# Kernel tuning notes

Hardware: AMD Instinct MI355X
Metric: run time of the kernel (lower is better)

The kernel has to match this reference:

```python
import jax, jax.numpy as jnp
import numpy as np

S, E, H, D, F = 2048, 1280, 16, 80, 5120
EPS = 1e-6


def _ln(x, g, b):
    m = x.mean(-1, keepdims=True)
    v = x.var(-1, keepdims=True)
    return (x - m) * jax.lax.rsqrt(v + EPS) * g + b


def _rotate_half(x):
    x1, x2 = jnp.split(x, 2, axis=-1)
    return jnp.concatenate([-x2, x1], axis=-1)


def _quick_gelu(x):
    return x * jax.nn.sigmoid(1.702 * x)


def setup_inputs() -> dict:
    key = jax.random.key(0)
    ks = jax.random.split(key, 12)
    inp = {
        "hidden_states": jax.random.normal(ks[0], (S, E), jnp.float32),
        "attention_mask": jnp.ones((1, 1, S, S), jnp.bool_),
        "cos": jax.random.uniform(ks[1], (S, D), jnp.float32),
        "sin": jax.random.uniform(ks[2], (S, D), jnp.float32),
        "ln1_g": jnp.ones((E,), jnp.float32),
        "ln1_b": jnp.zeros((E,), jnp.float32),
        "ln2_g": jnp.ones((E,), jnp.float32),
        "ln2_b": jnp.zeros((E,), jnp.float32),
        "w_qkv": jax.random.normal(ks[3], (E, 3 * E), jnp.float32) * (E ** -0.5),
        "b_qkv": jax.random.normal(ks[4], (3 * E,), jnp.float32) * 0.02,
        "w_o": jax.random.normal(ks[5], (E, E), jnp.float32) * (E ** -0.5),
        "b_o": jax.random.normal(ks[6], (E,), jnp.float32) * 0.02,
        "w_fc1": jax.random.normal(ks[7], (E, F), jnp.float32) * (E ** -0.5),
        "b_fc1": jax.random.normal(ks[8], (F,), jnp.float32) * 0.02,
        "w_fc2": jax.random.normal(ks[9], (F, E), jnp.float32) * (F ** -0.5),
        "b_fc2": jax.random.normal(ks[10], (E,), jnp.float32) * 0.02,
    }
    return inp


def reference(hidden_states, attention_mask, cos, sin, ln1_g, ln1_b, ln2_g, ln2_b,
              w_qkv, b_qkv, w_o, b_o, w_fc1, b_fc1, w_fc2, b_fc2):
    x = hidden_states  # [S, E]
    h = _ln(x, ln1_g, ln1_b)
    qkv = h @ w_qkv + b_qkv  # [S, 3E]
    q, k, v = jnp.split(qkv, 3, axis=-1)
    q = q.reshape(S, H, D)
    k = k.reshape(S, H, D)
    v = v.reshape(S, H, D)
    # rotary in fp32, cos/sin broadcast over head axis: [S, 1, D]
    c = cos[:, None, :].astype(jnp.float32)
    s = sin[:, None, :].astype(jnp.float32)
    qf, kf = q.astype(jnp.float32), k.astype(jnp.float32)
    q = (qf * c + _rotate_half(qf) * s).astype(q.dtype)
    k = (kf * c + _rotate_half(kf) * s).astype(k.dtype)
    # attention scores [H, S, S]
    scores = jnp.einsum('shd,thd->hst', q, k) / np.float32(np.sqrt(D))
    scores = jnp.where(attention_mask[0], scores, jnp.finfo(scores.dtype).min)
    probs = jax.nn.softmax(scores.astype(jnp.float32), axis=-1).astype(q.dtype)
    attn = jnp.einsum('hst,thd->shd', probs, v).reshape(S, E)
    attn = attn @ w_o + b_o
    x = x + attn
    h2 = _ln(x, ln2_g, ln2_b)
    mlp = _quick_gelu(h2 @ w_fc1 + b_fc1) @ w_fc2 + b_fc2
    return x + mlp
```

## Files before the change

kernel.cpp:

```cpp
#include <hip/hip_runtime.h>
#include <stdint.h>
#include <math.h>

#define S_LEN 2048
#define EMB   1280
#define NHEAD 16
#define HDIM  80
#define FDIM  5120

typedef __bf16 bf16x8 __attribute__((ext_vector_type(8)));
typedef float  f32x4  __attribute__((ext_vector_type(4)));
typedef int    i32x4  __attribute__((ext_vector_type(4)));
typedef unsigned short u16x8 __attribute__((ext_vector_type(8)));
typedef unsigned short u16x4 __attribute__((ext_vector_type(4)));

__device__ __forceinline__ float b2f(unsigned short u) {
    union { float f; unsigned int i; } x; x.i = ((unsigned int)u) << 16; return x.f;
}
__device__ __forceinline__ unsigned short f2b(float f) {
    union { float f; unsigned int i; } x; x.f = f;
    unsigned int r = x.i + 0x7FFFu + ((x.i >> 16) & 1u);
    return (unsigned short)(r >> 16);
}

__device__ __forceinline__ float wave_rsum(float v) {
    #pragma unroll
    for (int o = 32; o; o >>= 1) v += __shfl_down(v, o);
    return v;
}

__device__ __forceinline__ void trans64(
    const float* __restrict__ in, unsigned short* __restrict__ out,
    int R, int C, int bx, int by, int tid)
{
    __shared__ unsigned short tile[64][65];
    int c0 = bx * 64, r0 = by * 64;
    int tx = tid & 63, ty = tid >> 6;
    #pragma unroll
    for (int j = 0; j < 16; ++j) {
        int row = ty + j * 4;
        tile[row][tx] = f2b(in[(size_t)(r0 + row) * C + c0 + tx]);
    }
    __syncthreads();
    #pragma unroll
    for (int j = 0; j < 16; ++j) {
        int row = ty + j * 4;
        out[(size_t)(c0 + row) * R + r0 + tx] = tile[tx][row];
    }
}

__global__ __launch_bounds__(256) void transpose4_kernel(
    const float* __restrict__ w_qkv, unsigned short* __restrict__ wT_qkv,
    const float* __restrict__ w_o,   unsigned short* __restrict__ wT_o,
    const float* __restrict__ w_fc1, unsigned short* __restrict__ wT_fc1,
    const float* __restrict__ w_fc2, unsigned short* __restrict__ wT_fc2)
{
    int id = blockIdx.x, tid = threadIdx.x;
    if (id < 1200) {
        trans64(w_qkv, wT_qkv, 1280, 3840, id % 60, id / 60, tid);
    } else if (id < 1600) {
        int t = id - 1200;
        trans64(w_o, wT_o, 1280, 1280, t % 20, t / 20, tid);
    } else if (id < 3200) {
        int t = id - 1600;
        trans64(w_fc1, wT_fc1, 1280, 5120, t % 80, t / 80, tid);
    } else {
        int t = id - 3200;
        trans64(w_fc2, wT_fc2, 5120, 1280, t % 20, t / 20, tid);
    }
}

__global__ __launch_bounds__(256) void ln_kernel(
    const float* __restrict__ x,
    const float* __restrict__ g,
    const float* __restrict__ b,
    unsigned short* __restrict__ out)
{
    int row = blockIdx.x, tid = threadIdx.x;
    int lane = tid & 63, wave = tid >> 6;
    const float* xr = x + (size_t)row * EMB;
    float v[5], s = 0.f, ss = 0.f;
    #pragma unroll
    for (int i = 0; i < 5; ++i) {
        float f = xr[tid + i * 256];
        v[i] = f; s += f; ss += f * f;
    }
    s = wave_rsum(s); ss = wave_rsum(ss);
    __shared__ float rs[4], rss[4];
    if (lane == 0) { rs[wave] = s; rss[wave] = ss; }
    __syncthreads();
    float st  = rs[0] + rs[1] + rs[2] + rs[3];
    float sst = rss[0] + rss[1] + rss[2] + rss[3];
    float mean = st * (1.0f / EMB);
    float var  = sst * (1.0f / EMB) - mean * mean;
    float inv  = rsqrtf(var + 1e-6f);
    unsigned short* orow = out + (size_t)row * EMB;
    #pragma unroll
    for (int i = 0; i < 5; ++i) {
        int c = tid + i * 256;
        orow[c] = f2b((v[i] - mean) * inv * g[c] + b[c]);
    }
}

__global__ __launch_bounds__(256) void addbias_kernel(
    const float* __restrict__ res,
    const float* __restrict__ bias,
    float* __restrict__ out)
{
    size_t i4 = ((size_t)blockIdx.x * 256 + threadIdx.x) * 4;
    f32x4 a = *(const f32x4*)&res[i4];
    f32x4 bv = *(const f32x4*)&bias[(int)(i4 % EMB)];
    *(f32x4*)&out[i4] = a + bv;
}

template<int EPI, int OM, int SPLIT>
__global__ __launch_bounds__(256) void gemm_kernel(
    const unsigned short* __restrict__ A,
    const unsigned short* __restrict__ Bt,
    const float* __restrict__ bias,
    void* __restrict__ Cv,
    int M, int N, int K)
{
    __shared__ __align__(16) unsigned short As[2][128 * 32];
    __shared__ __align__(16) unsigned short Bs[2][128 * 32];

    int tid = threadIdx.x;
    int lane = tid & 63, wave = tid >> 6;

    int gx = gridDim.x, gy = gridDim.y;
    int nwg = gx * gy * gridDim.z;
    int flat = blockIdx.x + gx * (blockIdx.y + gy * blockIdx.z);
    int cpx = nwg >> 3;
    int logical = (flat & 7) * cpx + (flat >> 3);
    int bx = logical % gx;
    int rem = logical / gx;
    int by = rem % gy;
    int bz = rem / gy;

    int m0 = bx * 128, n0 = by * 128;
    int wm = (wave >> 1) * 64, wn = (wave & 1) * 64;
    int kc = K / SPLIT;
    int kbeg = bz * kc;
    const int NITER = kc / 32;

    f32x4 acc[4][4];
    #pragma unroll
    for (int i = 0; i < 4; ++i)
        #pragma unroll
        for (int j = 0; j < 4; ++j)
            acc[i][j] = (f32x4){0.f, 0.f, 0.f, 0.f};

    int u = tid ^ ((tid >> 3) & 7);
    const unsigned short* Ap0 = A  + (size_t)(m0 + (u >> 2)) * K + (u & 3) * 8 + kbeg;
    const unsigned short* Ap1 = Ap0 + (size_t)64 * K;
    const unsigned short* Bp0 = Bt + (size_t)(n0 + (u >> 2)) * K + (u & 3) * 8 + kbeg;
    const unsigned short* Bp1 = Bp0 + (size_t)64 * K;

    int arow = lane & 15, aq = (lane >> 4) * 8;
    int aswz = ((arow >> 1) & 7) << 3;
    int aoff[4], boff[4];
    #pragma unroll
    for (int i = 0; i < 4; ++i) {
        aoff[i] = ((wm + i * 16 + arow) * 32 + aq) ^ aswz;
        boff[i] = ((wn + i * 16 + arow) * 32 + aq) ^ aswz;
    }

    i32x4 rA0a, rA1a, rB0a, rB1a, rA0b, rA1b, rB0b, rB1b;

    rA0b = *(const i32x4*)(Ap0);
    rA1b = *(const i32x4*)(Ap1);
    rB0b = *(const i32x4*)(Bp0);
    rB1b = *(const i32x4*)(Bp1);
    *(i32x4*)&As[0][tid * 8]        = rA0b;
    *(i32x4*)&As[0][2048 + tid * 8] = rA1b;
    *(i32x4*)&Bs[0][tid * 8]        = rB0b;
    *(i32x4*)&Bs[0][2048 + tid * 8] = rB1b;
    if (NITER > 1) {
        rA0a = *(const i32x4*)(Ap0 + 32);
        rA1a = *(const i32x4*)(Ap1 + 32);
        rB0a = *(const i32x4*)(Bp0 + 32);
        rB1a = *(const i32x4*)(Bp1 + 32);
    }
    __syncthreads();

#define GSTEP(IT, AW0, AW1, BW0, BW1, AL0, AL1, BL0, BL1)                    \
    {                                                                         \
        const int cur = (IT) & 1, nb = cur ^ 1;                               \
        if ((IT) + 1 < NITER) {                                               \
            *(i32x4*)&As[nb][tid * 8]        = AW0;                           \
            *(i32x4*)&As[nb][2048 + tid * 8] = AW1;                           \
            *(i32x4*)&Bs[nb][tid * 8]        = BW0;                           \
            *(i32x4*)&Bs[nb][2048 + tid * 8] = BW1;                           \
        }                                                                     \
        if ((IT) + 2 < NITER) {                                               \
            int ko = ((IT) + 2) * 32;                                         \
            AL0 = *(const i32x4*)(Ap0 + ko);                                  \
            AL1 = *(const i32x4*)(Ap1 + ko);                                  \
            BL0 = *(const i32x4*)(Bp0 + ko);                                  \
            BL1 = *(const i32x4*)(Bp1 + ko);                                  \
        }                                                                     \
        bf16x8 af[4], bfm[4];                                                 \
        _Pragma("unroll") for (int i = 0; i < 4; ++i) {                       \
            af[i]  = *(const bf16x8*)&As[cur][aoff[i]];                       \
            bfm[i] = *(const bf16x8*)&Bs[cur][boff[i]];                       \
        }                                                                     \
        _Pragma("unroll") for (int mi = 0; mi < 4; ++mi)                      \
            _Pragma("unroll") for (int ni = 0; ni < 4; ++ni)                  \
                acc[mi][ni] = __builtin_amdgcn_mfma_f32_16x16x32_bf16(        \
                    af[mi], bfm[ni], acc[mi][ni], 0, 0, 0);                   \
        __syncthreads();                                                      \
    }

    for (int it = 0; it < NITER; it += 2) {
        GSTEP(it,     rA0a, rA1a, rB0a, rB1a, rA0b, rA1b, rB0b, rB1b)
        GSTEP(it + 1, rA0b, rA1b, rB0b, rB1b, rA0a, rA1a, rB0a, rB1a)
    }
#undef GSTEP

    int col = lane & 15;
    int rbase = (lane >> 4) * 4;
    #pragma unroll
    for (int ni = 0; ni < 4; ++ni) {
        int gn = n0 + wn + ni * 16 + col;
        float bv = (OM == 3) ? 0.f : bias[gn];
        #pragma unroll
        for (int mi = 0; mi < 4; ++mi) {
            int gm = m0 + wm + mi * 16 + rbase;
            #pragma unroll
            for (int r = 0; r < 4; ++r) {
                float v = acc[mi][ni][r] + bv;
                if (OM != 3) {
                    if (EPI == 1) v = v / (1.0f + expf(-1.702f * v));
                }
                if (OM == 3)
                    atomicAdd(&((float*)Cv)[(size_t)(gm + r) * N + gn], v);
                else if (OM == 1)
                    ((float*)Cv)[(size_t)(gm + r) * N + gn] = v;
                else
                    ((unsigned short*)Cv)[(size_t)(gm + r) * N + gn] = f2b(v);
            }
        }
    }
}

__global__ __launch_bounds__(256) void ropev_kernel(
    const unsigned short* __restrict__ qkv,
    const float* __restrict__ cosb,
    const float* __restrict__ sinb,
    unsigned short* __restrict__ q_out,
    unsigned short* __restrict__ k_out,
    unsigned short* __restrict__ vt)
{
    __shared__ unsigned short qT[64 * 84];
    __shared__ unsigned short kT[64 * 84];
    __shared__ unsigned short vT[64 * 84];

    int h = blockIdx.x >> 5, stile = blockIdx.x & 31;
    int s0 = stile * 64;
    int tid = threadIdx.x;

    u16x4 qr[5], kr[5];
    #pragma unroll
    for (int i = 0; i < 5; ++i) {
        int u = tid + i * 256;
        int row = u / 20, col = (u % 20) * 4;
        const unsigned short* base = qkv + (size_t)(s0 + row) * (3 * EMB) + h * HDIM + col;
        qr[i] = *(const u16x4*)base;
        kr[i] = *(const u16x4*)(base + EMB);
        u16x4 v4 = *(const u16x4*)(base + 2 * EMB);
        *(u16x4*)&qT[row * 84 + col] = qr[i];
        *(u16x4*)&kT[row * 84 + col] = kr[i];
        *(u16x4*)&vT[row * 84 + col] = v4;
    }
    __syncthreads();

    #pragma unroll
    for (int i = 0; i < 5; ++i) {
        int u = tid + i * 256;
        int row = u / 20, col = (u % 20) * 4;
        int pcol = (col < 40) ? col + 40 : col - 40;
        float sgn = (col < 40) ? -1.f : 1.f;
        u16x4 qp = *(const u16x4*)&qT[row * 84 + pcol];
        u16x4 kp = *(const u16x4*)&kT[row * 84 + pcol];
        f32x4 c4 = *(const f32x4*)&cosb[(size_t)(s0 + row) * HDIM + col];
        f32x4 s4 = *(const f32x4*)&sinb[(size_t)(s0 + row) * HDIM + col];
        u16x4 qo, ko;
        #pragma unroll
        for (int j = 0; j < 4; ++j) {
            qo[j] = f2b(b2f(qr[i][j]) * c4[j] + sgn * b2f(qp[j]) * s4[j]);
            ko[j] = f2b(b2f(kr[i][j]) * c4[j] + sgn * b2f(kp[j]) * s4[j]);
        }
        size_t o = ((size_t)h * S_LEN + s0 + row) * HDIM + col;
        *(u16x4*)&q_out[o] = qo;
        *(u16x4*)&k_out[o] = ko;
    }
    #pragma unroll
    for (int i = 0; i < 5; ++i) {
        int w = tid + i * 256;
        int d = w >> 4, c4i = (w & 15) * 4;
        u16x4 pk;
        #pragma unroll
        for (int j = 0; j < 4; ++j) pk[j] = vT[(c4i + j) * 84 + d];
        *(u16x4*)(vt + ((size_t)h * HDIM + d) * S_LEN + s0 + c4i) = pk;
    }
}

__global__ __launch_bounds__(256) void fattn_kernel(
    const unsigned short* __restrict__ q,
    const unsigned short* __restrict__ k,
    const unsigned short* __restrict__ vt,
    unsigned short* __restrict__ out)
{
    __shared__ __align__(16) unsigned short Ks[2][64 * 96];
    __shared__ __align__(16) unsigned short Vs[2][80 * 72];
    __shared__ __align__(16) unsigned short Pt[4 * 16 * 72];

    int tid = threadIdx.x;
    int lane = tid & 63, wave = tid >> 6;
    int arow = lane & 15, quad = lane >> 4;
    int logical = (blockIdx.x & 7) * 64 + (blockIdx.x >> 3);
    int h = logical >> 5, qb = logical & 31;
    int s0 = qb * 64;
    const float c = 0.16129856f;

    const unsigned short* kbase = k + (size_t)h * S_LEN * HDIM;
    const unsigned short* vbase = vt + (size_t)h * HDIM * S_LEN;

    bf16x8 qf[3];
    {
        const unsigned short* qrp =
            q + ((size_t)h * S_LEN + s0 + wave * 16 + arow) * HDIM;
        #pragma unroll
        for (int kk = 0; kk < 3; ++kk) {
            int col = kk * 32 + quad * 8;
            u16x8 qv = (u16x8){0, 0, 0, 0, 0, 0, 0, 0};
            if (col < HDIM) qv = *(const u16x8*)(qrp + col);
            u16x8 qs8;
            #pragma unroll
            for (int j = 0; j < 8; ++j) qs8[j] = f2b(b2f(qv[j]) * c);
            qf[kk] = *(bf16x8*)&qs8;
        }
    }

    {
        int zr = tid >> 2, zc = 80 + (tid & 3) * 4;
        int zidx = (zr * 96 + zc) ^ ((zr & 7) << 3);
        *(u16x4*)&Ks[0][zidx] = (u16x4){0, 0, 0, 0};
        *(u16x4*)&Ks[1][zidx] = (u16x4){0, 0, 0, 0};
    }

    u16x4 kreg[5], vreg[5];
    #pragma unroll
    for (int i = 0; i < 5; ++i) {
        int u = tid + i * 256;
        kreg[i] = *(const u16x4*)(kbase + u * 4);
        vreg[i] = *(const u16x4*)(vbase + (size_t)(u >> 4) * S_LEN + (u & 15) * 4);
    }
    #pragma unroll
    for (int i = 0; i < 5; ++i) {
        int u = tid + i * 256;
        int row = u / 20, c4 = (u % 20) * 4;
        *(u16x4*)&Ks[0][(row * 96 + c4) ^ ((row & 7) << 3)] = kreg[i];
        *(u16x4*)&Vs[0][(u >> 4) * 72 + (u & 15) * 4] = vreg[i];
    }
    #pragma unroll
    for (int i = 0; i < 5; ++i) {
        int u = tid + i * 256;
        kreg[i] = *(const u16x4*)(kbase + (size_t)64 * HDIM + u * 4);
        vreg[i] = *(const u16x4*)(vbase + (size_t)(u >> 4) * S_LEN + 64 + (u & 15) * 4);
    }
    __syncthreads();

    int ksw[3];
    #pragma unroll
    for (int kk = 0; kk < 3; ++kk)
        ksw[kk] = (arow * 96 + kk * 32 + quad * 8) ^ ((arow & 7) << 3);

    int pw = wave * 16 * 72;
    int poff = pw + arow * 72 + ((arow >> 3) << 2);

    float l_part = 0.f;
    f32x4 o[5];
    #pragma unroll
    for (int di = 0; di < 5; ++di) o[di] = (f32x4){0.f, 0.f, 0.f, 0.f};

    const int NIT = S_LEN / 64;
    for (int it = 0; it < NIT; ++it) {
        int cur = it & 1;
        if (it + 1 < NIT) {
            int nb = (it + 1) & 1;
            #pragma unroll
            for (int i = 0; i < 5; ++i) {
                int u = tid + i * 256;
                int row = u / 20, c4 = (u % 20) * 4;
                *(u16x4*)&Ks[nb][(row * 96 + c4) ^ ((row & 7) << 3)] = kreg[i];
                *(u16x4*)&Vs[nb][(u >> 4) * 72 + (u & 15) * 4] = vreg[i];
            }
        }
        if (it + 2 < NIT) {
            int t0 = (it + 2) * 64;
            #pragma unroll
            for (int i = 0; i < 5; ++i) {
                int u = tid + i * 256;
                kreg[i] = *(const u16x4*)(kbase + (size_t)t0 * HDIM + u * 4);
                vreg[i] = *(const u16x4*)(vbase + (size_t)(u >> 4) * S_LEN + t0 + (u & 15) * 4);
            }
        }

        f32x4 sc[4];
        #pragma unroll
        for (int ni = 0; ni < 4; ++ni) sc[ni] = (f32x4){0.f, 0.f, 0.f, 0.f};
        __builtin_amdgcn_s_setprio(1);
        #pragma unroll
        for (int kk = 0; kk < 3; ++kk) {
            bf16x8 bq = qf[kk];
            #pragma unroll
            for (int ni = 0; ni < 4; ++ni) {
                bf16x8 ak = *(const bf16x8*)&Ks[cur][ksw[kk] + ni * 1536];
                sc[ni] = __builtin_amdgcn_mfma_f32_16x16x32_bf16(ak, bq, sc[ni], 0, 0, 0);
            }
        }
        __builtin_amdgcn_s_setprio(0);

        #pragma unroll
        for (int ni = 0; ni < 4; ++ni) {
            u16x4 pk;
            #pragma unroll
            for (int r = 0; r < 4; ++r) {
                float p = __builtin_amdgcn_exp2f(sc[ni][r]);
                l_part += p;
                __bf16 pb = (__bf16)p;
                pk[r] = *(unsigned short*)&pb;
            }
            *(u16x4*)&Pt[poff + ni * 16 + quad * 4] = pk;
        }

        __builtin_amdgcn_s_setprio(1);
        #pragma unroll
        for (int kk = 0; kk < 2; ++kk) {
            u16x4 plo = *(const u16x4*)&Pt[poff + kk * 32 + quad * 8];
            u16x4 phi = *(const u16x4*)&Pt[poff + kk * 32 + quad * 8 + 4];
            u16x8 apu = (u16x8){plo[0], plo[1], plo[2], plo[3],
                                phi[0], phi[1], phi[2], phi[3]};
            bf16x8 ap = *(bf16x8*)&apu;
            #pragma unroll
            for (int di = 0; di < 5; ++di) {
                bf16x8 bv = *(const bf16x8*)&Vs[cur][(di * 16 + arow) * 72 + kk * 32 + quad * 8];
                o[di] = __builtin_amdgcn_mfma_f32_16x16x32_bf16(ap, bv, o[di], 0, 0, 0);
            }
        }
        __builtin_amdgcn_s_setprio(0);

        __syncthreads();
    }

    float l_run = l_part;
    l_run += __shfl_xor(l_run, 16);
    l_run += __shfl_xor(l_run, 32);

    float inv[4];
    #pragma unroll
    for (int r = 0; r < 4; ++r)
        inv[r] = 1.f / __shfl(l_run, (lane & 48) | (quad * 4 + r));
    #pragma unroll
    for (int r = 0; r < 4; ++r) {
        int gq = s0 + wave * 16 + quad * 4 + r;
        unsigned short* op = out + (size_t)gq * EMB + h * HDIM;
        #pragma unroll
        for (int di = 0; di < 5; ++di)
            op[di * 16 + arow] = f2b(o[di][r] * inv[r]);
    }
}

extern "C" void kernel_launch(void* const* d_in, const int* in_sizes, int n_in,
                              void* d_out, int out_size, void* d_ws, size_t ws_size,
                              hipStream_t stream)
{
    const float* hidden = (const float*)d_in[0];
    const float* cosb  = (const float*)d_in[2];
    const float* sinb  = (const float*)d_in[3];
    const float* ln1g  = (const float*)d_in[4];
    const float* ln1b  = (const float*)d_in[5];
    const float* ln2g  = (const float*)d_in[6];
    const float* ln2b  = (const float*)d_in[7];
    const float* w_qkv = (const float*)d_in[8];
    const float* b_qkv = (const float*)d_in[9];
    const float* w_o   = (const float*)d_in[10];
    const float* b_o   = (const float*)d_in[11];
    const float* w_fc1 = (const float*)d_in[12];
    const float* b_fc1 = (const float*)d_in[13];
    const float* w_fc2 = (const float*)d_in[14];
    const float* b_fc2 = (const float*)d_in[15];

    char* ws = (char*)d_ws;
    size_t off = 0;
    auto alloc = [&](size_t bytes) -> void* {
        void* p = (void*)(ws + off);
        off += (bytes + 255) & ~(size_t)255;
        return p;
    };
    unsigned short* wT_qkv = (unsigned short*)alloc((size_t)3840 * 1280 * 2);
    unsigned short* wT_o   = (unsigned short*)alloc((size_t)1280 * 1280 * 2);
    unsigned short* wT_fc1 = (unsigned short*)alloc((size_t)5120 * 1280 * 2);
    unsigned short* wT_fc2 = (unsigned short*)alloc((size_t)1280 * 5120 * 2);
    unsigned short* h1     = (unsigned short*)alloc((size_t)S_LEN * EMB * 2);
    unsigned short* qkv    = (unsigned short*)alloc((size_t)S_LEN * 3 * EMB * 2);
    unsigned short* q_r    = (unsigned short*)alloc((size_t)S_LEN * EMB * 2);
    unsigned short* k_r    = (unsigned short*)alloc((size_t)S_LEN * EMB * 2);
    unsigned short* vt_g   = (unsigned short*)alloc((size_t)S_LEN * EMB * 2);
    unsigned short* attn_o = (unsigned short*)alloc((size_t)S_LEN * EMB * 2);
    float*          x1     = (float*)alloc((size_t)S_LEN * EMB * 4);
    unsigned short* h2     = (unsigned short*)alloc((size_t)S_LEN * EMB * 2);
    unsigned short* mlp1   = (unsigned short*)alloc((size_t)S_LEN * FDIM * 2);

    transpose4_kernel<<<4800, 256, 0, stream>>>(
        w_qkv, wT_qkv, w_o, wT_o, w_fc1, wT_fc1, w_fc2, wT_fc2);

    ln_kernel<<<S_LEN, 256, 0, stream>>>(hidden, ln1g, ln1b, h1);

    gemm_kernel<0, 0, 1><<<dim3(S_LEN / 128, 3840 / 128, 1), 256, 0, stream>>>(
        h1, wT_qkv, b_qkv, qkv, S_LEN, 3 * EMB, EMB);

    ropev_kernel<<<NHEAD * (S_LEN / 64), 256, 0, stream>>>(qkv, cosb, sinb, q_r, k_r, vt_g);

    fattn_kernel<<<NHEAD * (S_LEN / 64), 256, 0, stream>>>(q_r, k_r, vt_g, attn_o);

    addbias_kernel<<<(S_LEN * EMB / 4) / 256, 256, 0, stream>>>(hidden, b_o, x1);
    gemm_kernel<0, 3, 2><<<dim3(S_LEN / 128, 1280 / 128, 2), 256, 0, stream>>>(
        attn_o, wT_o, nullptr, x1, S_LEN, EMB, EMB);

    ln_kernel<<<S_LEN, 256, 0, stream>>>(x1, ln2g, ln2b, h2);

    gemm_kernel<1, 0, 1><<<dim3(S_LEN / 128, FDIM / 128, 1), 256, 0, stream>>>(
        h2, wT_fc1, b_fc1, mlp1, S_LEN, FDIM, EMB);

    addbias_kernel<<<(S_LEN * EMB / 4) / 256, 256, 0, stream>>>(x1, b_fc2, (float*)d_out);
    gemm_kernel<0, 3, 4><<<dim3(S_LEN / 128, 1280 / 128, 4), 256, 0, stream>>>(
        mlp1, wT_fc2, nullptr, (float*)d_out, S_LEN, EMB, FDIM);
}
```

Measured before the change: 378.8 us.

## Replace split-K atomics with partial buffers and fuse reduction into LayerNorm

The split-K output-projection and FC2 GEMMs now write per-split fp32 partials instead of doing atomicAdd into a pre-biased buffer. A new kernel sums the two attention partials with the residual and bias and applies LayerNorm 2 in the same pass. A separate kernel reduces the four FC2 partials with the residual and bias. This removes the addbias kernels, the atomic traffic and a separate LN launch, at the cost of extra partial-buffer writes and reads, and the partials reuse the earlier workspace regions starting at h1.

```diff
diff --git a/kernel.cpp b/kernel.cpp
--- a/kernel.cpp
+++ b/kernel.cpp
@@ -102,15 +102,64 @@
     }
 }
 
-__global__ __launch_bounds__(256) void addbias_kernel(
+__global__ __launch_bounds__(256) void reduce2ln_kernel(
+    const float* __restrict__ part,
+    const float* __restrict__ res,
+    const float* __restrict__ bias,
+    const float* __restrict__ g,
+    const float* __restrict__ b,
+    float* __restrict__ x_out,
+    unsigned short* __restrict__ h_out)
+{
+    int row = blockIdx.x, tid = threadIdx.x;
+    int lane = tid & 63, wave = tid >> 6;
+    const size_t slice = (size_t)S_LEN * EMB;
+    const float* p0 = part + (size_t)row * EMB;
+    const float* p1 = p0 + slice;
+    const float* rr = res + (size_t)row * EMB;
+    float v[5], s = 0.f, ss = 0.f;
+    #pragma unroll
+    for (int i = 0; i < 5; ++i) {
+        int c = tid + i * 256;
+        float f = rr[c] + bias[c] + p0[c] + p1[c];
+        v[i] = f; s += f; ss += f * f;
+    }
+    s = wave_rsum(s); ss = wave_rsum(ss);
+    __shared__ float rs[4], rss[4];
+    if (lane == 0) { rs[wave] = s; rss[wave] = ss; }
+    __syncthreads();
+    float st  = rs[0] + rs[1] + rs[2] + rs[3];
+    float sst = rss[0] + rss[1] + rss[2] + rss[3];
+    float mean = st * (1.0f / EMB);
+    float var  = sst * (1.0f / EMB) - mean * mean;
+    float inv  = rsqrtf(var + 1e-6f);
+    float* xrow = x_out + (size_t)row * EMB;
+    unsigned short* hrow = h_out + (size_t)row * EMB;
+    #pragma unroll
+    for (int i = 0; i < 5; ++i) {
+        int c = tid + i * 256;
+        xrow[c] = v[i];
+        hrow[c] = f2b((v[i] - mean) * inv * g[c] + b[c]);
+    }
+}
+
+template<int Z>
+__global__ __launch_bounds__(256) void reduceZ_kernel(
+    const float* __restrict__ part,
     const float* __restrict__ res,
     const float* __restrict__ bias,
     float* __restrict__ out)
 {
     size_t i4 = ((size_t)blockIdx.x * 256 + threadIdx.x) * 4;
+    int colb = (int)(i4 % EMB);
     f32x4 a = *(const f32x4*)&res[i4];
-    f32x4 bv = *(const f32x4*)&bias[(int)(i4 % EMB)];
-    *(f32x4*)&out[i4] = a + bv;
+    f32x4 bv = *(const f32x4*)&bias[colb];
+    a += bv;
+    const size_t slice = (size_t)S_LEN * EMB;
+    #pragma unroll
+    for (int z = 0; z < Z; ++z)
+        a += *(const f32x4*)&part[z * slice + i4];
+    *(f32x4*)&out[i4] = a;
 }
 
 template<int EPI, int OM, int SPLIT>
@@ -222,20 +271,18 @@
     #pragma unroll
     for (int ni = 0; ni < 4; ++ni) {
         int gn = n0 + wn + ni * 16 + col;
-        float bv = (OM == 3) ? 0.f : bias[gn];
+        float bv = (OM == 2) ? 0.f : bias[gn];
         #pragma unroll
         for (int mi = 0; mi < 4; ++mi) {
             int gm = m0 + wm + mi * 16 + rbase;
             #pragma unroll
             for (int r = 0; r < 4; ++r) {
                 float v = acc[mi][ni][r] + bv;
-                if (OM != 3) {
+                if (OM != 2) {
                     if (EPI == 1) v = v / (1.0f + expf(-1.702f * v));
                 }
-                if (OM == 3)
-                    atomicAdd(&((float*)Cv)[(size_t)(gm + r) * N + gn], v);
-                else if (OM == 1)
-                    ((float*)Cv)[(size_t)(gm + r) * N + gn] = v;
+                if (OM == 2)
+                    ((float*)Cv)[((size_t)bz * M + gm + r) * N + gn] = v;
                 else
                     ((unsigned short*)Cv)[(size_t)(gm + r) * N + gn] = f2b(v);
             }
@@ -512,6 +559,7 @@
     float*          x1     = (float*)alloc((size_t)S_LEN * EMB * 4);
     unsigned short* h2     = (unsigned short*)alloc((size_t)S_LEN * EMB * 2);
     unsigned short* mlp1   = (unsigned short*)alloc((size_t)S_LEN * FDIM * 2);
+    float* partials = (float*)h1;
 
     transpose4_kernel<<<4800, 256, 0, stream>>>(
         w_qkv, wT_qkv, w_o, wT_o, w_fc1, wT_fc1, w_fc2, wT_fc2);
@@ -525,16 +573,16 @@
 
     fattn_kernel<<<NHEAD * (S_LEN / 64), 256, 0, stream>>>(q_r, k_r, vt_g, attn_o);
 
-    addbias_kernel<<<(S_LEN * EMB / 4) / 256, 256, 0, stream>>>(hidden, b_o, x1);
-    gemm_kernel<0, 3, 2><<<dim3(S_LEN / 128, 1280 / 128, 2), 256, 0, stream>>>(
-        attn_o, wT_o, nullptr, x1, S_LEN, EMB, EMB);
-
-    ln_kernel<<<S_LEN, 256, 0, stream>>>(x1, ln2g, ln2b, h2);
+    gemm_kernel<0, 2, 2><<<dim3(S_LEN / 128, 1280 / 128, 2), 256, 0, stream>>>(
+        attn_o, wT_o, nullptr, partials, S_LEN, EMB, EMB);
+    reduce2ln_kernel<<<S_LEN, 256, 0, stream>>>(
+        partials, hidden, b_o, ln2g, ln2b, x1, h2);
 
     gemm_kernel<1, 0, 1><<<dim3(S_LEN / 128, FDIM / 128, 1), 256, 0, stream>>>(
         h2, wT_fc1, b_fc1, mlp1, S_LEN, FDIM, EMB);
 
-    addbias_kernel<<<(S_LEN * EMB / 4) / 256, 256, 0, stream>>>(x1, b_fc2, (float*)d_out);
-    gemm_kernel<0, 3, 4><<<dim3(S_LEN / 128, 1280 / 128, 4), 256, 0, stream>>>(
-        mlp1, wT_fc2, nullptr, (float*)d_out, S_LEN, EMB, FDIM);
-}
+    gemm_kernel<0, 2, 4><<<dim3(S_LEN / 128, 1280 / 128, 4), 256, 0, stream>>>(
+        mlp1, wT_fc2, nullptr, partials, S_LEN, EMB, FDIM);
+    reduceZ_kernel<4><<<(S_LEN * EMB / 4) / 256, 256, 0, stream>>>(
+        partials, x1, b_fc2, (float*)d_out);
+}
```

Result: faster. 351.9 us (-7.1%).
